# Kernel tuning notes

Measured on AMD Instinct MI355X. Metric: run time of the kernel, lower is better.

## Reference

```python
import jax, jax.numpy as jnp
import numpy as np

NEG_INF = -9e15
ALPHA = 0.2  # LeakyReLU negative slope

N = 8192
D_IN = 512
D_OUT = 256


def setup_inputs() -> dict:
    key = jax.random.key(0)
    k1, k2, k3, k4, k5 = jax.random.split(key, 5)
    features = jax.random.normal(k1, (N, D_IN), dtype=jnp.float32)
    adjacency_matrix = jax.random.randint(k2, (N, N), 0, 2, dtype=jnp.int32)
    # learned params (torch Linear stores [out, in]; we use [in, out] layout)
    s_phi = 1.0 / np.sqrt(D_IN)
    W_phi = jax.random.uniform(k3, (D_IN, D_OUT), jnp.float32, -s_phi, s_phi)
    s_v = 1.0 / np.sqrt(D_OUT)
    w_mu = jax.random.uniform(k4, (D_OUT,), jnp.float32, -s_v, s_v)
    w_xi = jax.random.uniform(k5, (D_OUT,), jnp.float32, -s_v, s_v)
    return {"features": features, "adjacency_matrix": adjacency_matrix,
            "W_phi": W_phi, "w_mu": w_mu, "w_xi": w_xi}


def reference(features, adjacency_matrix, W_phi, w_mu, w_xi):
    h = features @ W_phi                                   # [N, d_out]
    mu = h @ w_mu                                          # [N]
    xi = h @ w_xi                                          # [N]
    e = mu[:, None] + xi[None, :]                          # [N, N] additive scores
    e = jnp.where(e >= 0, e, ALPHA * e)                    # LeakyReLU
    e = jnp.where(adjacency_matrix > 0, e, NEG_INF)        # mask non-edges
    a = jax.nn.softmax(e, axis=1)                          # row softmax (dropout p=0)
    out = a @ h                                            # weighted aggregation
    return jax.nn.elu(out)
```

## Files before the change

### kernel.cpp

```cpp
#include <hip/hip_runtime.h>
#include <cstdint>
#include <cstddef>


#define LOG2E 1.44269504f

typedef __attribute__((ext_vector_type(8))) short short8;
typedef __attribute__((ext_vector_type(4))) float floatx4;

using uint_as1 = __attribute__((address_space(1))) unsigned int;
using uint_as3 = __attribute__((address_space(3))) unsigned int;

__device__ __forceinline__ void gld_lds16(const void* g, void* l) {
  __builtin_amdgcn_global_load_lds((const uint_as1*)g, (uint_as3*)l, 16, 0, 0);
}

__device__ __forceinline__ unsigned short f2b(float f) {
  unsigned u = __float_as_uint(f);
  u += 0x7fffu + ((u >> 16) & 1u);
  return (unsigned short)(u >> 16);
}
__device__ __forceinline__ float b2f(short s) {
  return __uint_as_float(((unsigned)(unsigned short)s) << 16);
}

__global__ void k_bitmaskz(const int* __restrict__ adj,
                           const float* __restrict__ Emu, const float* __restrict__ Fmu,
                           const float* __restrict__ Exi, const float* __restrict__ Fxi,
                           unsigned long long* __restrict__ bm, float* __restrict__ zbuf) {
  int gw = (blockIdx.x * 256 + threadIdx.x) >> 6;
  int lane = threadIdx.x & 63;
  float EM = Emu[gw], FM = Fmu[gw];
  size_t w0 = (size_t)gw * 128;
  float z = 0.f;
  for (int r = 0; r < 128; r += 4) {
    size_t wd = w0 + r;
    int v0 = adj[(wd + 0) * 64 + lane];
    int v1 = adj[(wd + 1) * 64 + lane];
    int v2 = adj[(wd + 2) * 64 + lane];
    int v3 = adj[(wd + 3) * 64 + lane];
    float e0 = Exi[(r + 0) * 64 + lane], f0 = Fxi[(r + 0) * 64 + lane];
    float e1 = Exi[(r + 1) * 64 + lane], f1 = Fxi[(r + 1) * 64 + lane];
    float e2 = Exi[(r + 2) * 64 + lane], f2 = Fxi[(r + 2) * 64 + lane];
    float e3 = Exi[(r + 3) * 64 + lane], f3 = Fxi[(r + 3) * 64 + lane];
    unsigned long long m0 = __ballot(v0 != 0);
    unsigned long long m1 = __ballot(v1 != 0);
    unsigned long long m2 = __ballot(v2 != 0);
    unsigned long long m3 = __ballot(v3 != 0);
    z += (v0 != 0) ? fmaxf(EM * e0, FM * f0) : 0.f;
    z += (v1 != 0) ? fmaxf(EM * e1, FM * f1) : 0.f;
    z += (v2 != 0) ? fmaxf(EM * e2, FM * f2) : 0.f;
    z += (v3 != 0) ? fmaxf(EM * e3, FM * f3) : 0.f;
    if (lane == 0) {
      bm[wd] = m0; bm[wd + 1] = m1; bm[wd + 2] = m2; bm[wd + 3] = m3;
    }
  }
#pragma unroll
  for (int off = 32; off > 0; off >>= 1) z += __shfl_xor(z, off);
  if (lane == 0) zbuf[gw] = z;
}

__global__ void k_cvt_features(const float* __restrict__ f, unsigned short* __restrict__ fb) {
  int tid = blockIdx.x * 256 + threadIdx.x;
  float4 v = ((const float4*)f)[tid];
  ushort4 o = {f2b(v.x), f2b(v.y), f2b(v.z), f2b(v.w)};
  *(ushort4*)&fb[tid * 4] = o;
}

__global__ void k_prep_wt(const float* __restrict__ w, unsigned short* __restrict__ wt) {
  int tid = blockIdx.x * 256 + threadIdx.x;
  int n = tid >> 9, k = tid & 511;
  wt[n * 512 + k] = f2b(w[k * 256 + n]);
}

__global__ void k_prep_p(const float* __restrict__ w, const float* __restrict__ wmu,
                         const float* __restrict__ wxi, float* __restrict__ pmu,
                         float* __restrict__ pxi) {
  int tid = blockIdx.x * 256 + threadIdx.x;
  int k = tid >> 2, seg = tid & 3;
  float sm = 0.f, sx = 0.f;
  int base = k * 256 + seg * 64;
#pragma unroll
  for (int c = 0; c < 64; c += 4) {
    float4 wv = *(const float4*)&w[base + c];
    float4 mv = *(const float4*)&wmu[seg * 64 + c];
    float4 xv = *(const float4*)&wxi[seg * 64 + c];
    sm += wv.x * mv.x + wv.y * mv.y + wv.z * mv.z + wv.w * mv.w;
    sx += wv.x * xv.x + wv.y * xv.y + wv.z * xv.z + wv.w * xv.w;
  }
  sm += __shfl_xor(sm, 1); sm += __shfl_xor(sm, 2);
  sx += __shfl_xor(sx, 1); sx += __shfl_xor(sx, 2);
  if (seg == 0) { pmu[k] = sm; pxi[k] = sx; }
}

__global__ void k_mu_xi(const unsigned short* __restrict__ fb, const float* __restrict__ pmu,
                        const float* __restrict__ pxi, float* __restrict__ Emu,
                        float* __restrict__ Fmu, float* __restrict__ Exi,
                        float* __restrict__ Fxi) {
  int w = threadIdx.x >> 6, l = threadIdx.x & 63;
  int i = blockIdx.x * 4 + w;
  short8 fv = *(const short8*)&fb[i * 512 + l * 8];
  float m = 0.f, x = 0.f;
#pragma unroll
  for (int c = 0; c < 8; ++c) {
    float fvf = b2f(fv[c]);
    m = fmaf(fvf, pmu[l * 8 + c], m);
    x = fmaf(fvf, pxi[l * 8 + c], x);
  }
#pragma unroll
  for (int off = 32; off > 0; off >>= 1) {
    m += __shfl_xor(m, off);
    x += __shfl_xor(x, off);
  }
  if (l == 0) {
    float ms = m * LOG2E, xs = x * LOG2E;
    Emu[i] = __builtin_amdgcn_exp2f(ms);
    Fmu[i] = __builtin_amdgcn_exp2f(0.2f * ms);
    Exi[i] = __builtin_amdgcn_exp2f(xs);
    Fxi[i] = __builtin_amdgcn_exp2f(0.2f * xs);
  }
}

__global__ __launch_bounds__(256, 2) void k_gemm1(const unsigned short* __restrict__ fb,
                                                  const unsigned short* __restrict__ wt,
                                                  unsigned short* __restrict__ ht) {
  __shared__ __align__(16) unsigned short As[64 * 64];
  __shared__ __align__(16) unsigned short Bs[128 * 64];
  int t = threadIdx.x, w = t >> 6, l = t & 63;
  int bm_ = blockIdx.x >> 1, bn = blockIdx.x & 1;
  int m0 = bm_ * 64, n0 = bn * 128;
  int lr = l >> 3, lg = l & 7, g = lg ^ lr;
  int kg = l >> 4, ln = l & 15;
  floatx4 zero = {0.f, 0.f, 0.f, 0.f};
  floatx4 acc[4][2];
#pragma unroll
  for (int mf = 0; mf < 4; ++mf)
#pragma unroll
    for (int nf = 0; nf < 2; ++nf) acc[mf][nf] = zero;

  for (int it = 0; it < 8; ++it) {
    int k0 = it * 64;
#pragma unroll
    for (int q = 0; q < 2; ++q) {
      int row = w * 16 + q * 8 + lr;
      const void* gp = fb + (size_t)(m0 + row) * 512 + k0 + g * 8;
      int lb = __builtin_amdgcn_readfirstlane((w * 16 + q * 8) * 64);
      gld_lds16(gp, &As[lb]);
    }
#pragma unroll
    for (int q = 0; q < 4; ++q) {
      int row = w * 32 + q * 8 + lr;
      const void* gp = wt + (size_t)(n0 + row) * 512 + k0 + g * 8;
      int lb = __builtin_amdgcn_readfirstlane((w * 32 + q * 8) * 64);
      gld_lds16(gp, &Bs[lb]);
    }
    __syncthreads();
#pragma unroll
    for (int ks = 0; ks < 2; ++ks) {
      int gg = ks * 4 + kg;
      int swz = (gg ^ (ln & 7)) * 8;
      short8 bfr[2];
#pragma unroll
      for (int nf = 0; nf < 2; ++nf)
        bfr[nf] = *(const short8*)&Bs[(w * 32 + nf * 16 + ln) * 64 + swz];
#pragma unroll
      for (int mf = 0; mf < 4; ++mf) {
        short8 afr = *(const short8*)&As[(mf * 16 + ln) * 64 + swz];
#pragma unroll
        for (int nf = 0; nf < 2; ++nf)
          acc[mf][nf] = __builtin_amdgcn_mfma_f32_16x16x32_bf16(afr, bfr[nf], acc[mf][nf], 0, 0, 0);
      }
    }
    __syncthreads();
  }
#pragma unroll
  for (int mf = 0; mf < 4; ++mf)
#pragma unroll
    for (int nf = 0; nf < 2; ++nf) {
      int ng = n0 + w * 32 + nf * 16 + ln;
      int mg = m0 + mf * 16 + kg * 4;
      ushort4 o = {f2b(acc[mf][nf][0]), f2b(acc[mf][nf][1]),
                   f2b(acc[mf][nf][2]), f2b(acc[mf][nf][3])};
      *(ushort4*)&ht[(size_t)ng * 8192 + mg] = o;
    }
}

__global__ __launch_bounds__(512, 2) void k_gatt5(const unsigned char* __restrict__ bm8,
                                                  const unsigned short* __restrict__ ht,
                                                  const float* __restrict__ Emu,
                                                  const float* __restrict__ Fmu,
                                                  const float* __restrict__ Exi,
                                                  const float* __restrict__ Fxi,
                                                  float* __restrict__ nump) {
  __shared__ __align__(16) unsigned short Bs[2][256 * 64];
  __shared__ __align__(16) unsigned char BitAll[256 * 128];
  __shared__ __align__(16) float EfE[1024];
  __shared__ __align__(16) float EfF[1024];

  int t = threadIdx.x, w = t >> 6, l = t & 63;
  int ln = l & 15, kg = l >> 4;
  int jb = blockIdx.x & 7, ig = blockIdx.x >> 3;
  int i0 = ig * 256;
  int jc0 = jb * 1024;

  if (t < 256) {
    *(float4*)&EfE[t * 4] = *(const float4*)&Exi[jc0 + t * 4];
  } else {
    int t2 = t - 256;
    *(float4*)&EfF[t2 * 4] = *(const float4*)&Fxi[jc0 + t2 * 4];
  }
#pragma unroll
  for (int r = 0; r < 4; ++r) {
    int c = r * 512 + t;
    int row = c >> 3, gp_ = c & 7;
    int g = gp_ ^ (row & 7);
    const void* src = bm8 + (size_t)(i0 + row) * 1024 + jb * 128 + g * 16;
    int lb = __builtin_amdgcn_readfirstlane((r * 512 + w * 64) * 16);
    gld_lds16(src, &BitAll[lb]);
  }

  float EM[2], FM[2];
#pragma unroll
  for (int mf = 0; mf < 2; ++mf) {
    int i = i0 + w * 32 + mf * 16 + ln;
    EM[mf] = Emu[i];
    FM[mf] = Fmu[i];
  }

  floatx4 zero = {0.f, 0.f, 0.f, 0.f};
  floatx4 acc[2][16];
#pragma unroll
  for (int mf = 0; mf < 2; ++mf)
#pragma unroll
    for (int nf = 0; nf < 16; ++nf) acc[mf][nf] = zero;

#define STAGE(hw_, b_)                                                        \
  {                                                                           \
    int j0_ = jc0 + (hw_) * 64;                                               \
    _Pragma("unroll")                                                         \
    for (int q = 0; q < 4; ++q) {                                             \
      int r0 = w * 32 + q * 8;                                                \
      int row = r0 + (l >> 3);                                                \
      int g = (l & 7) ^ (row & 7);                                            \
      const void* gp = ht + (size_t)row * 8192 + j0_ + g * 8;                 \
      int lb = __builtin_amdgcn_readfirstlane((b_) * (256 * 64) + r0 * 64);   \
      gld_lds16(gp, &Bs[0][lb]);                                              \
    }                                                                         \
  }

  STAGE(0, 0);
  __syncthreads();

  for (int hw = 0; hw < 16; ++hw) {
    int buf = hw & 1;
    if (hw < 15) STAGE(hw + 1, buf ^ 1);

    unsigned long long bw[2];
#pragma unroll
    for (int mf = 0; mf < 2; ++mf) {
      int rowL = w * 32 + mf * 16 + ln;
      bw[mf] = *(const unsigned long long*)
          &BitAll[rowL * 128 + (((hw >> 1) ^ (rowL & 7)) * 16) + (hw & 1) * 8];
    }

#pragma unroll
    for (int ksl = 0; ksl < 2; ++ksl) {
      int gran = ksl * 4 + kg;
      int jl = hw * 64 + gran * 8;
      float4 e0 = *(const float4*)&EfE[jl];
      float4 e1 = *(const float4*)&EfE[jl + 4];
      float4 f0 = *(const float4*)&EfF[jl];
      float4 f1 = *(const float4*)&EfF[jl + 4];
      float ex[8] = {e0.x, e0.y, e0.z, e0.w, e1.x, e1.y, e1.z, e1.w};
      float fx[8] = {f0.x, f0.y, f0.z, f0.w, f1.x, f1.y, f1.z, f1.w};
      short8 af[2];
#pragma unroll
      for (int mf = 0; mf < 2; ++mf) {
        unsigned bits = (unsigned)(bw[mf] >> ((ksl * 4 + kg) * 8)) & 0xffu;
        float A = EM[mf], F = FM[mf];
#pragma unroll
        for (int e = 0; e < 8; ++e) {
          float m = fmaxf(A * ex[e], F * fx[e]);
          m = (bits & (1u << e)) ? m : 0.f;
          af[mf][e] = (short)f2b(m);
        }
      }
#pragma unroll
      for (int half = 0; half < 2; ++half) {
        short8 bfv[8];
#pragma unroll
        for (int nf = 0; nf < 8; ++nf) {
          int n = half * 128 + nf * 16 + ln;
          bfv[nf] = *(const short8*)&Bs[buf][n * 64 + ((gran ^ (n & 7)) * 8)];
        }
#pragma unroll
        for (int mf = 0; mf < 2; ++mf)
#pragma unroll
          for (int nf = 0; nf < 8; ++nf)
            acc[mf][half * 8 + nf] = __builtin_amdgcn_mfma_f32_16x16x32_bf16(
                af[mf], bfv[nf], acc[mf][half * 8 + nf], 0, 0, 0);
      }
    }
    __syncthreads();
  }
#undef STAGE

  float* np = nump + (size_t)jb * (8192 * 256);
#pragma unroll
  for (int mf = 0; mf < 2; ++mf) {
    int rowb = i0 + w * 32 + mf * 16 + kg * 4;
#pragma unroll
    for (int r = 0; r < 4; ++r) {
      float* rp = np + (size_t)(rowb + r) * 256;
#pragma unroll
      for (int nf = 0; nf < 16; ++nf)
        rp[nf * 16 + ln] = acc[mf][nf][r];
    }
  }
}

__global__ void k_final(const float* __restrict__ nump, const float* __restrict__ zbuf,
                        float* __restrict__ out) {
  int tid = blockIdx.x * 256 + threadIdx.x;
  int i = tid >> 6;
  float zi = 1.0f / zbuf[i];
  float4 v = {0.f, 0.f, 0.f, 0.f};
#pragma unroll
  for (int p = 0; p < 8; ++p) {
    float4 s = *(const float4*)&nump[(size_t)p * (8192 * 256) + tid * 4];
    v.x += s.x; v.y += s.y; v.z += s.z; v.w += s.w;
  }
  v.x *= zi; v.y *= zi; v.z *= zi; v.w *= zi;
  v.x = (v.x > 0.f) ? v.x : (__builtin_amdgcn_exp2f(v.x * LOG2E) - 1.f);
  v.y = (v.y > 0.f) ? v.y : (__builtin_amdgcn_exp2f(v.y * LOG2E) - 1.f);
  v.z = (v.z > 0.f) ? v.z : (__builtin_amdgcn_exp2f(v.z * LOG2E) - 1.f);
  v.w = (v.w > 0.f) ? v.w : (__builtin_amdgcn_exp2f(v.w * LOG2E) - 1.f);
  *(float4*)&out[tid * 4] = v;
}

extern "C" void kernel_launch(void* const* d_in, const int* in_sizes, int n_in,
                              void* d_out, int out_size, void* d_ws, size_t ws_size,
                              hipStream_t stream) {
  const float* features = (const float*)d_in[0];
  const int* adjm = (const int*)d_in[1];
  const float* W_phi = (const float*)d_in[2];
  const float* w_mu = (const float*)d_in[3];
  const float* w_xi = (const float*)d_in[4];
  float* out = (float*)d_out;

  char* ws = (char*)d_ws;
  unsigned short* fb  = (unsigned short*)(ws + 0);
  unsigned short* ht  = (unsigned short*)(ws + 8388608);
  unsigned short* wt  = (unsigned short*)(ws + 12582912);
  float* pmu = (float*)(ws + 12845056);
  float* pxi = (float*)(ws + 12847104);
  float* Emu = (float*)(ws + 12849152);
  float* Fmu = (float*)(ws + 12881920);
  float* Exi = (float*)(ws + 12914688);
  float* Fxi = (float*)(ws + 12947456);
  float* zbuf = (float*)(ws + 12980224);
  unsigned char* bmask = (unsigned char*)(ws + 13631488);
  float* nump = (float*)(ws + 25165824);

  k_cvt_features<<<4096, 256, 0, stream>>>(features, fb);
  k_prep_wt<<<512, 256, 0, stream>>>(W_phi, wt);
  k_prep_p<<<8, 256, 0, stream>>>(W_phi, w_mu, w_xi, pmu, pxi);
  k_mu_xi<<<2048, 256, 0, stream>>>(fb, pmu, pxi, Emu, Fmu, Exi, Fxi);
  k_gemm1<<<256, 256, 0, stream>>>(fb, wt, ht);
  k_bitmaskz<<<2048, 256, 0, stream>>>(adjm, Emu, Fmu, Exi, Fxi,
                                       (unsigned long long*)bmask, zbuf);
  k_gatt5<<<256, 512, 0, stream>>>(bmask, ht, Emu, Fmu, Exi, Fxi, nump);
  k_final<<<2048, 256, 0, stream>>>(nump, zbuf, out);
}
```

Baseline: 471.0 us.

## Widen staged K-window to 128 and prefetch adjacency bits into registers

The attention aggregation kernel now stages 128-column windows of the transposed h tile per double-buffer step instead of 64, halving the number of barrier-separated iterations. The adjacency bitmask is no longer preloaded into shared memory; each lane reads its row's 16-byte bit word straight from global memory, prefetched one window ahead into registers. This frees LDS for the larger B buffers (LDS use rises from about 160KB to about 136KB+ per block pair) and removes the bitmask LDS traffic. In exchange it adds uncoalesced per-lane global loads and more register pressure under the 2-blocks-per-CU launch bound.

```diff
diff --git a/kernel.cpp b/kernel.cpp
--- a/kernel.cpp
+++ b/kernel.cpp
@@ -185,15 +185,14 @@
     }
 }
 
-__global__ __launch_bounds__(512, 2) void k_gatt5(const unsigned char* __restrict__ bm8,
+__global__ __launch_bounds__(512, 2) void k_gatt6(const unsigned char* __restrict__ bm8,
                                                   const unsigned short* __restrict__ ht,
                                                   const float* __restrict__ Emu,
                                                   const float* __restrict__ Fmu,
                                                   const float* __restrict__ Exi,
                                                   const float* __restrict__ Fxi,
                                                   float* __restrict__ nump) {
-  __shared__ __align__(16) unsigned short Bs[2][256 * 64];
-  __shared__ __align__(16) unsigned char BitAll[256 * 128];
+  __shared__ __align__(16) unsigned short Bs[2][256 * 128];
   __shared__ __align__(16) float EfE[1024];
   __shared__ __align__(16) float EfF[1024];
 
@@ -209,22 +208,15 @@
     int t2 = t - 256;
     *(float4*)&EfF[t2 * 4] = *(const float4*)&Fxi[jc0 + t2 * 4];
   }
-#pragma unroll
-  for (int r = 0; r < 4; ++r) {
-    int c = r * 512 + t;
-    int row = c >> 3, gp_ = c & 7;
-    int g = gp_ ^ (row & 7);
-    const void* src = bm8 + (size_t)(i0 + row) * 1024 + jb * 128 + g * 16;
-    int lb = __builtin_amdgcn_readfirstlane((r * 512 + w * 64) * 16);
-    gld_lds16(src, &BitAll[lb]);
-  }
 
   float EM[2], FM[2];
+  const uint4* bprow[2];
 #pragma unroll
   for (int mf = 0; mf < 2; ++mf) {
     int i = i0 + w * 32 + mf * 16 + ln;
     EM[mf] = Emu[i];
     FM[mf] = Fmu[i];
+    bprow[mf] = (const uint4*)(bm8 + (size_t)i * 1024 + jb * 128);
   }
 
   floatx4 zero = {0.f, 0.f, 0.f, 0.f};
@@ -234,39 +226,37 @@
 #pragma unroll
     for (int nf = 0; nf < 16; ++nf) acc[mf][nf] = zero;
 
-#define STAGE(hw_, b_)                                                        \
+#define STAGE(win_, b_)                                                       \
   {                                                                           \
-    int j0_ = jc0 + (hw_) * 64;                                               \
+    int j0_ = jc0 + (win_) * 128;                                             \
     _Pragma("unroll")                                                         \
-    for (int q = 0; q < 4; ++q) {                                             \
-      int r0 = w * 32 + q * 8;                                                \
-      int row = r0 + (l >> 3);                                                \
-      int g = (l & 7) ^ (row & 7);                                            \
+    for (int q = 0; q < 8; ++q) {                                             \
+      int r0 = w * 32 + q * 4;                                                \
+      int row = r0 + (l >> 4);                                                \
+      int g = (l & 15) ^ (row & 15);                                          \
       const void* gp = ht + (size_t)row * 8192 + j0_ + g * 8;                 \
-      int lb = __builtin_amdgcn_readfirstlane((b_) * (256 * 64) + r0 * 64);   \
+      int lb = __builtin_amdgcn_readfirstlane((b_) * (256 * 128) + r0 * 128); \
       gld_lds16(gp, &Bs[0][lb]);                                              \
     }                                                                         \
   }
 
+  uint4 bc[2], bnx[2];
+#pragma unroll
+  for (int mf = 0; mf < 2; ++mf) bc[mf] = bprow[mf][0];
   STAGE(0, 0);
   __syncthreads();
 
-  for (int hw = 0; hw < 16; ++hw) {
-    int buf = hw & 1;
-    if (hw < 15) STAGE(hw + 1, buf ^ 1);
-
-    unsigned long long bw[2];
-#pragma unroll
-    for (int mf = 0; mf < 2; ++mf) {
-      int rowL = w * 32 + mf * 16 + ln;
-      bw[mf] = *(const unsigned long long*)
-          &BitAll[rowL * 128 + (((hw >> 1) ^ (rowL & 7)) * 16) + (hw & 1) * 8];
-    }
-
-#pragma unroll
-    for (int ksl = 0; ksl < 2; ++ksl) {
+  for (int win = 0; win < 8; ++win) {
+    int buf = win & 1;
+    if (win < 7) {
+      STAGE(win + 1, buf ^ 1);
+#pragma unroll
+      for (int mf = 0; mf < 2; ++mf) bnx[mf] = bprow[mf][win + 1];
+    }
+#pragma unroll
+    for (int ksl = 0; ksl < 4; ++ksl) {
       int gran = ksl * 4 + kg;
-      int jl = hw * 64 + gran * 8;
+      int jl = win * 128 + gran * 8;
       float4 e0 = *(const float4*)&EfE[jl];
       float4 e1 = *(const float4*)&EfE[jl + 4];
       float4 f0 = *(const float4*)&EfF[jl];
@@ -276,7 +266,9 @@
       short8 af[2];
 #pragma unroll
       for (int mf = 0; mf < 2; ++mf) {
-        unsigned bits = (unsigned)(bw[mf] >> ((ksl * 4 + kg) * 8)) & 0xffu;
+        unsigned word = (ksl == 0) ? bc[mf].x : (ksl == 1) ? bc[mf].y
+                      : (ksl == 2) ? bc[mf].z : bc[mf].w;
+        unsigned bits = (word >> (kg * 8)) & 0xffu;
         float A = EM[mf], F = FM[mf];
 #pragma unroll
         for (int e = 0; e < 8; ++e) {
@@ -291,7 +283,7 @@
 #pragma unroll
         for (int nf = 0; nf < 8; ++nf) {
           int n = half * 128 + nf * 16 + ln;
-          bfv[nf] = *(const short8*)&Bs[buf][n * 64 + ((gran ^ (n & 7)) * 8)];
+          bfv[nf] = *(const short8*)&Bs[buf][n * 128 + ((gran ^ (n & 15)) * 8)];
         }
 #pragma unroll
         for (int mf = 0; mf < 2; ++mf)
@@ -302,6 +294,8 @@
       }
     }
     __syncthreads();
+#pragma unroll
+    for (int mf = 0; mf < 2; ++mf) bc[mf] = bnx[mf];
   }
 #undef STAGE
 
@@ -369,6 +363,6 @@
   k_gemm1<<<256, 256, 0, stream>>>(fb, wt, ht);
   k_bitmaskz<<<2048, 256, 0, stream>>>(adjm, Emu, Fmu, Exi, Fxi,
                                        (unsigned long long*)bmask, zbuf);
-  k_gatt5<<<256, 512, 0, stream>>>(bmask, ht, Emu, Fmu, Exi, Fxi, nump);
+  k_gatt6<<<256, 512, 0, stream>>>(bmask, ht, Emu, Fmu, Exi, Fxi, nump);
   k_final<<<2048, 256, 0, stream>>>(nump, zbuf, out);
 }
```

After: 465.7 us. About the same (-1.1%).
